# Performance work log

Measured on AMD Instinct MI355X. Metric: run time of the kernel, lower is better.

Reference implementation:

```python
import jax, jax.numpy as jnp
import numpy as np

T, B, I, H, O = 512, 64, 256, 512, 256

def setup_inputs() -> dict:
    key = jax.random.key(0)
    ks = jax.random.split(key, 7)
    s_ih = 1.0 / np.sqrt(H)
    return {
        "inputs": jax.random.normal(ks[0], (T, B, I), dtype=jnp.float32),
        "W_ih": jax.random.uniform(ks[1], (4 * H, I), minval=-s_ih, maxval=s_ih, dtype=jnp.float32),
        "W_hh": jax.random.uniform(ks[2], (4 * H, H), minval=-s_ih, maxval=s_ih, dtype=jnp.float32),
        "b_ih": jax.random.uniform(ks[3], (4 * H,), minval=-s_ih, maxval=s_ih, dtype=jnp.float32),
        "b_hh": jax.random.uniform(ks[4], (4 * H,), minval=-s_ih, maxval=s_ih, dtype=jnp.float32),
        "W_out": jax.random.uniform(ks[5], (O, H), minval=-s_ih, maxval=s_ih, dtype=jnp.float32),
        "b_out": jax.random.uniform(ks[6], (O,), minval=-s_ih, maxval=s_ih, dtype=jnp.float32),
    }

def reference(inputs, W_ih, W_hh, b_ih, b_hh, W_out, b_out):
    Bsz = inputs.shape[1]
    Hd = W_hh.shape[1]
    h0 = jnp.zeros((Bsz, Hd), dtype=inputs.dtype)
    c0 = jnp.zeros((Bsz, Hd), dtype=inputs.dtype)
    # Precompute input contribution for all timesteps in one big GEMM: [T,B,4H]
    x_gates = jnp.einsum('tbi,gi->tbg', inputs, W_ih) + b_ih + b_hh

    def step(carry, xg):
        h, c = carry
        gates = xg + h @ W_hh.T  # [B,4H]
        i, f, g, o = jnp.split(gates, 4, axis=-1)  # PyTorch LSTMCell gate order
        i = jax.nn.sigmoid(i)
        f = jax.nn.sigmoid(f)
        g = jnp.tanh(g)
        o = jax.nn.sigmoid(o)
        c_new = f * c + i * g
        h_new = o * jnp.tanh(c_new)
        return (h_new, c_new), h_new

    (h_T, c_T), hs = jax.lax.scan(step, (h0, c0), x_gates)
    # Output projection over all timesteps at once: [T,B,O]
    outputs = jnp.einsum('tbh,oh->tbo', hs, W_out) + b_out
    return (outputs, h_T, c_T)
```

## Files before the change

kernel.cpp:

```cpp
#include <hip/hip_runtime.h>
#include <hip/hip_bf16.h>

#define TLEN 512
#define BATCH 64
#define ISZ 256
#define HSZ 512
#define OSZ 256
#define G4 2048

typedef float f32x4 __attribute__((ext_vector_type(4)));
typedef short short8 __attribute__((ext_vector_type(8)));
typedef int int4v __attribute__((ext_vector_type(4)));

#define MFMA(a, b, c) __builtin_amdgcn_mfma_f32_16x16x32_bf16((a), (b), (c), 0, 0, 0)

__device__ __forceinline__ unsigned short f2bf(float x) {
    unsigned int u = __float_as_uint(x);
    u = (u + 0x7fffu + ((u >> 16) & 1u)) >> 16;
    return (unsigned short)u;
}
__device__ __forceinline__ float bf2f(unsigned short h) {
    return __uint_as_float(((unsigned int)h) << 16);
}
__device__ __forceinline__ float sigmoidf_(float x) { return 1.0f / (1.0f + __expf(-x)); }
__device__ __forceinline__ float tanhf_(float x) { return 1.0f - 2.0f / (__expf(2.0f * x) + 1.0f); }

__global__ void __launch_bounds__(512, 1) xg_gemm(
    const float* __restrict__ inp, const float* __restrict__ Wih,
    const float* __restrict__ b_ih, const float* __restrict__ b_hh,
    unsigned short* __restrict__ xg)
{
    __shared__ short8 blds[8][8][64];
    const int tid = threadIdx.x;
    {
        int row = tid >> 2;
        int kseg = (tid & 3) * 64;
        int nt = row >> 4, nn = row & 15;
        const float* src = Wih + (size_t)(blockIdx.y * 128 + row) * ISZ + kseg;
        for (int kk = 0; kk < 64; ++kk) {
            int k = kseg + kk;
            int kf = k >> 5, sub = k & 31;
            ((unsigned short*)&blds[nt][kf][((sub >> 3) << 4) | nn])[sub & 7] = f2bf(src[kk]);
        }
    }
    __syncthreads();
    const int wave = tid >> 6, lane = tid & 63;
    const int m0 = blockIdx.x * 128 + wave * 16;
    f32x4 acc[8];
    #pragma unroll
    for (int i = 0; i < 8; ++i) acc[i] = (f32x4){0.f, 0.f, 0.f, 0.f};
    const float* arow = inp + (size_t)(m0 + (lane & 15)) * ISZ + ((lane >> 4) * 8);
    #pragma unroll
    for (int kf = 0; kf < 8; ++kf) {
        f32x4 a0 = *(const f32x4*)(arow + kf * 32);
        f32x4 a1 = *(const f32x4*)(arow + kf * 32 + 4);
        short8 af;
        #pragma unroll
        for (int i = 0; i < 4; ++i) { af[i] = (short)f2bf(a0[i]); af[4 + i] = (short)f2bf(a1[i]); }
        #pragma unroll
        for (int nt = 0; nt < 8; ++nt)
            acc[nt] = MFMA(af, blds[nt][kf][lane], acc[nt]);
    }
    const int nn = lane & 15;
    #pragma unroll
    for (int nt = 0; nt < 8; ++nt) {
        int nc = blockIdx.y * 128 + nt * 16 + nn;
        float bias = b_ih[nc] + b_hh[nc];
        #pragma unroll
        for (int r = 0; r < 4; ++r) {
            int m = m0 + (lane >> 4) * 4 + r;
            xg[(size_t)m * G4 + nc] = f2bf(acc[nt][r] + bias);
        }
    }
}

__global__ void __attribute__((amdgpu_waves_per_eu(1, 1))) __launch_bounds__(256, 1) lstm_scan(
    const float* __restrict__ Whh, const unsigned short* __restrict__ xg,
    unsigned short* __restrict__ hs, unsigned int* __restrict__ hbuf,
    float* __restrict__ out_tail)
{
    __shared__ short8 wlds[4][16][64];
    const int wg = blockIdx.x, tid = threadIdx.x;
    const int wave = tid >> 6, lane = tid & 63;
    const int l15 = lane & 15, l4 = lane >> 4;
    const int col = wg * 16 + l15;

    {
        const int g = wave;
        const float* wrow = Whh + (size_t)(g * HSZ + wg * 16 + l15) * HSZ + l4 * 8;
        #pragma unroll
        for (int kf = 0; kf < 16; ++kf) {
            f32x4 w0 = *(const f32x4*)(wrow + kf * 32);
            f32x4 w1 = *(const f32x4*)(wrow + kf * 32 + 4);
            short8 f;
            #pragma unroll
            for (int e = 0; e < 4; ++e) { f[e] = (short)f2bf(w0[e]); f[4 + e] = (short)f2bf(w1[e]); }
            wlds[g][kf][lane] = f;
        }
    }
    __syncthreads();

    float cr[4] = {0.f, 0.f, 0.f, 0.f};
    const int mbase = wave * 16 + l4 * 4;

    #pragma unroll 1
    for (int t = 0; t < TLEN; ++t) {
        unsigned int xgv[4][4];
        {
            const char* x0 = (const char*)(xg + (size_t)(t * BATCH + mbase) * G4 + col);
            #pragma unroll
            for (int r = 0; r < 4; ++r) {
                const char* xr = x0 + r * (G4 * 2);
                asm volatile("global_load_ushort %0, %1, off offset:0"    : "=v"(xgv[0][r]) : "v"(xr));
                asm volatile("global_load_ushort %0, %1, off offset:1024" : "=v"(xgv[1][r]) : "v"(xr));
                asm volatile("global_load_ushort %0, %1, off offset:2048" : "=v"(xgv[2][r]) : "v"(xr));
                asm volatile("global_load_ushort %0, %1, off offset:3072" : "=v"(xgv[3][r]) : "v"(xr));
            }
        }

        f32x4 acc[4];
        #pragma unroll
        for (int g = 0; g < 4; ++g) acc[g] = (f32x4){0.f, 0.f, 0.f, 0.f};

        if (t > 0) {
            const unsigned tag = (unsigned)t;
            const char* hb = (const char*)hbuf + (t & 1) * 131072
                           + (size_t)(wave * 16 + l15) * 2048 + l4 * 32;
            int4v hv[32];
            while (true) {
                #pragma unroll
                for (int kf = 0; kf < 16; ++kf) {
                    asm volatile("global_load_dwordx4 %0, %1, off offset:%2 sc0 sc1"
                                 : "=&v"(hv[2 * kf])     : "v"(hb), "i"(kf * 128));
                    asm volatile("global_load_dwordx4 %0, %1, off offset:%2 sc0 sc1"
                                 : "=&v"(hv[2 * kf + 1]) : "v"(hb), "i"(kf * 128 + 16));
                }
                asm volatile("s_waitcnt vmcnt(0)" ::: "memory");
                __builtin_amdgcn_sched_barrier(0);
                unsigned bad = 0;
                #pragma unroll
                for (int w = 0; w < 32; ++w) {
                    bad |= (unsigned)(hv[w][0] ^ (int)tag);
                    bad |= (unsigned)(hv[w][1] ^ (int)tag);
                    bad |= (unsigned)(hv[w][2] ^ (int)tag);
                    bad |= (unsigned)(hv[w][3] ^ (int)tag);
                }
                if (__all((bad & 0xFFFFu) == 0)) break;
            }
            __builtin_amdgcn_sched_barrier(0);
            #pragma unroll
            for (int kf = 0; kf < 16; ++kf) {
                int4v w0 = hv[2 * kf], w1 = hv[2 * kf + 1];
                int4v f;
                f[0] = (int)(((unsigned)w0[0] >> 16) | ((unsigned)w0[1] & 0xFFFF0000u));
                f[1] = (int)(((unsigned)w0[2] >> 16) | ((unsigned)w0[3] & 0xFFFF0000u));
                f[2] = (int)(((unsigned)w1[0] >> 16) | ((unsigned)w1[1] & 0xFFFF0000u));
                f[3] = (int)(((unsigned)w1[2] >> 16) | ((unsigned)w1[3] & 0xFFFF0000u));
                short8 a = *(short8*)&f;
                acc[0] = MFMA(a, wlds[0][kf][lane], acc[0]);
                acc[1] = MFMA(a, wlds[1][kf][lane], acc[1]);
                acc[2] = MFMA(a, wlds[2][kf][lane], acc[2]);
                acc[3] = MFMA(a, wlds[3][kf][lane], acc[3]);
            }
        }
        asm volatile("s_waitcnt vmcnt(0)" ::: "memory");
        __builtin_amdgcn_sched_barrier(0);

        float hnv[4];
        #pragma unroll
        for (int r = 0; r < 4; ++r) {
            float iv = acc[0][r] + bf2f((unsigned short)xgv[0][r]);
            float fv2= acc[1][r] + bf2f((unsigned short)xgv[1][r]);
            float gv = acc[2][r] + bf2f((unsigned short)xgv[2][r]);
            float ov = acc[3][r] + bf2f((unsigned short)xgv[3][r]);
            float si = sigmoidf_(iv), sf = sigmoidf_(fv2), so = sigmoidf_(ov);
            float tg = tanhf_(gv);
            float cn = sf * cr[r] + si * tg;
            cr[r] = cn;
            hnv[r] = so * tanhf_(cn);
        }

        {
            const unsigned ptag = (unsigned)(t + 1);
            const unsigned pbase = ((unsigned)((t + 1) & 1)) * 32768u + (unsigned)col;
            #pragma unroll
            for (int r = 0; r < 4; ++r) {
                unsigned word = (((unsigned)f2bf(hnv[r])) << 16) | ptag;
                __hip_atomic_store(&hbuf[pbase + (unsigned)(mbase + r) * 512], word,
                                   __ATOMIC_RELAXED, __HIP_MEMORY_SCOPE_AGENT);
            }
        }

        #pragma unroll
        for (int r = 0; r < 4; ++r) {
            int m = mbase + r;
            hs[((size_t)t * BATCH + m) * HSZ + col] = f2bf(hnv[r]);
            if (t == TLEN - 1) {
                out_tail[(size_t)m * HSZ + col] = hnv[r];
                out_tail[(size_t)BATCH * HSZ + (size_t)m * HSZ + col] = cr[r];
            }
        }
    }
}

__global__ void __launch_bounds__(512, 1) out_gemm(
    const unsigned short* __restrict__ hs, const float* __restrict__ Wout,
    const float* __restrict__ b_out, float* __restrict__ out)
{
    __shared__ short8 blds[4][16][64];
    const int tid = threadIdx.x;
    {
        int row = tid >> 3;
        int kseg = (tid & 7) * 64;
        int nt = row >> 4, nn = row & 15;
        const float* src = Wout + (size_t)(blockIdx.y * 64 + row) * HSZ + kseg;
        for (int kk = 0; kk < 64; ++kk) {
            int k = kseg + kk;
            int kf = k >> 5, sub = k & 31;
            ((unsigned short*)&blds[nt][kf][((sub >> 3) << 4) | nn])[sub & 7] = f2bf(src[kk]);
        }
    }
    __syncthreads();
    const int wave = tid >> 6, lane = tid & 63;
    const int m0 = blockIdx.x * 128 + wave * 16;
    f32x4 acc[4];
    #pragma unroll
    for (int i = 0; i < 4; ++i) acc[i] = (f32x4){0.f, 0.f, 0.f, 0.f};
    const unsigned short* arow = hs + (size_t)(m0 + (lane & 15)) * HSZ + ((lane >> 4) * 8);
    #pragma unroll
    for (int kf = 0; kf < 16; ++kf) {
        short8 a = *(const short8*)(arow + kf * 32);
        #pragma unroll
        for (int nt = 0; nt < 4; ++nt)
            acc[nt] = MFMA(a, blds[nt][kf][lane], acc[nt]);
    }
    const int nn = lane & 15;
    #pragma unroll
    for (int nt = 0; nt < 4; ++nt) {
        int nc = blockIdx.y * 64 + nt * 16 + nn;
        float bias = b_out[nc];
        #pragma unroll
        for (int r = 0; r < 4; ++r) {
            int m = m0 + (lane >> 4) * 4 + r;
            out[(size_t)m * OSZ + nc] = acc[nt][r] + bias;
        }
    }
}

extern "C" void kernel_launch(void* const* d_in, const int* in_sizes, int n_in,
                              void* d_out, int out_size, void* d_ws, size_t ws_size,
                              hipStream_t stream)
{
    const float* inputs = (const float*)d_in[0];
    const float* W_ih  = (const float*)d_in[1];
    const float* W_hh  = (const float*)d_in[2];
    const float* b_ih  = (const float*)d_in[3];
    const float* b_hh  = (const float*)d_in[4];
    const float* W_out = (const float*)d_in[5];
    const float* b_out = (const float*)d_in[6];
    float* out = (float*)d_out;

    char* ws = (char*)d_ws;
    unsigned short* xg = (unsigned short*)ws;
    unsigned short* hs = (unsigned short*)(ws + 134217728);
    unsigned int* hbuf = (unsigned int*)(ws + 134217728 + 33554432);

    xg_gemm<<<dim3(256, 16), 512, 0, stream>>>(inputs, W_ih, b_ih, b_hh, xg);

    float* out_tail = out + (size_t)TLEN * BATCH * OSZ;
    const float* whh_p = W_hh;
    const unsigned short* xg_p = xg;
    unsigned short* hs_p = hs;
    unsigned int* hbuf_p = hbuf;
    float* tail_p = out_tail;
    void* scan_args[] = { &whh_p, &xg_p, &hs_p, &hbuf_p, &tail_p };
    hipLaunchCooperativeKernel((void*)lstm_scan, dim3(32), dim3(256), scan_args, 0, stream);

    out_gemm<<<dim3(256, 4), 512, 0, stream>>>(hs, W_out, b_out, out);
}
```

Before: 4.105 ms.

## Re-layout xg gate buffer per column for vectorized loads and trim tag checks

```diff
diff --git a/kernel.cpp b/kernel.cpp
--- a/kernel.cpp
+++ b/kernel.cpp
@@ -10,6 +10,7 @@
 
 typedef float f32x4 __attribute__((ext_vector_type(4)));
 typedef short short8 __attribute__((ext_vector_type(8)));
+typedef int int2v __attribute__((ext_vector_type(2)));
 typedef int int4v __attribute__((ext_vector_type(4)));
 
 #define MFMA(a, b, c) __builtin_amdgcn_mfma_f32_16x16x32_bf16((a), (b), (c), 0, 0, 0)
@@ -62,15 +63,17 @@
             acc[nt] = MFMA(af, blds[nt][kf][lane], acc[nt]);
     }
     const int nn = lane & 15;
+    const int mf = m0 + (lane >> 4) * 4;
+    const int tt = mf >> 6, bb = mf & 63;
     #pragma unroll
     for (int nt = 0; nt < 8; ++nt) {
         int nc = blockIdx.y * 128 + nt * 16 + nn;
         float bias = b_ih[nc] + b_hh[nc];
-        #pragma unroll
-        for (int r = 0; r < 4; ++r) {
-            int m = m0 + (lane >> 4) * 4 + r;
-            xg[(size_t)m * G4 + nc] = f2bf(acc[nt][r] + bias);
-        }
+        int colc = nc & 511, gate = nc >> 9;
+        unsigned lo = (unsigned)f2bf(acc[nt][0] + bias) | ((unsigned)f2bf(acc[nt][1] + bias) << 16);
+        unsigned hi = (unsigned)f2bf(acc[nt][2] + bias) | ((unsigned)f2bf(acc[nt][3] + bias) << 16);
+        int2v w; w[0] = (int)lo; w[1] = (int)hi;
+        *(int2v*)((char*)xg + (size_t)(tt * 512 + colc) * 512 + gate * 128 + bb * 2) = w;
     }
 }
 
@@ -105,17 +108,16 @@
 
     #pragma unroll 1
     for (int t = 0; t < TLEN; ++t) {
-        unsigned int xgv[4][4];
+        int2v xv[4];
         {
-            const char* x0 = (const char*)(xg + (size_t)(t * BATCH + mbase) * G4 + col);
-            #pragma unroll
-            for (int r = 0; r < 4; ++r) {
-                const char* xr = x0 + r * (G4 * 2);
-                asm volatile("global_load_ushort %0, %1, off offset:0"    : "=v"(xgv[0][r]) : "v"(xr));
-                asm volatile("global_load_ushort %0, %1, off offset:1024" : "=v"(xgv[1][r]) : "v"(xr));
-                asm volatile("global_load_ushort %0, %1, off offset:2048" : "=v"(xgv[2][r]) : "v"(xr));
-                asm volatile("global_load_ushort %0, %1, off offset:3072" : "=v"(xgv[3][r]) : "v"(xr));
-            }
+            const char* xb = (const char*)xg + (size_t)(t * 512 + col) * 512 + mbase * 2;
+            asm volatile(
+                "global_load_dwordx2 %0, %4, off offset:0\n\t"
+                "global_load_dwordx2 %1, %4, off offset:128\n\t"
+                "global_load_dwordx2 %2, %4, off offset:256\n\t"
+                "global_load_dwordx2 %3, %4, off offset:384"
+                : "=&v"(xv[0]), "=&v"(xv[1]), "=&v"(xv[2]), "=&v"(xv[3])
+                : "v"(xb) : "memory");
         }
 
         f32x4 acc[4];
@@ -128,23 +130,54 @@
                            + (size_t)(wave * 16 + l15) * 2048 + l4 * 32;
             int4v hv[32];
             while (true) {
-                #pragma unroll
-                for (int kf = 0; kf < 16; ++kf) {
-                    asm volatile("global_load_dwordx4 %0, %1, off offset:%2 sc0 sc1"
-                                 : "=&v"(hv[2 * kf])     : "v"(hb), "i"(kf * 128));
-                    asm volatile("global_load_dwordx4 %0, %1, off offset:%2 sc0 sc1"
-                                 : "=&v"(hv[2 * kf + 1]) : "v"(hb), "i"(kf * 128 + 16));
-                }
+                asm volatile(
+                    "global_load_dwordx4 %0, %32, off offset:0 sc0 sc1\n\t"
+                    "global_load_dwordx4 %1, %32, off offset:16 sc0 sc1\n\t"
+                    "global_load_dwordx4 %2, %32, off offset:128 sc0 sc1\n\t"
+                    "global_load_dwordx4 %3, %32, off offset:144 sc0 sc1\n\t"
+                    "global_load_dwordx4 %4, %32, off offset:256 sc0 sc1\n\t"
+                    "global_load_dwordx4 %5, %32, off offset:272 sc0 sc1\n\t"
+                    "global_load_dwordx4 %6, %32, off offset:384 sc0 sc1\n\t"
+                    "global_load_dwordx4 %7, %32, off offset:400 sc0 sc1\n\t"
+                    "global_load_dwordx4 %8, %32, off offset:512 sc0 sc1\n\t"
+                    "global_load_dwordx4 %9, %32, off offset:528 sc0 sc1\n\t"
+                    "global_load_dwordx4 %10, %32, off offset:640 sc0 sc1\n\t"
+                    "global_load_dwordx4 %11, %32, off offset:656 sc0 sc1\n\t"
+                    "global_load_dwordx4 %12, %32, off offset:768 sc0 sc1\n\t"
+                    "global_load_dwordx4 %13, %32, off offset:784 sc0 sc1\n\t"
+                    "global_load_dwordx4 %14, %32, off offset:896 sc0 sc1\n\t"
+                    "global_load_dwordx4 %15, %32, off offset:912 sc0 sc1\n\t"
+                    "global_load_dwordx4 %16, %32, off offset:1024 sc0 sc1\n\t"
+                    "global_load_dwordx4 %17, %32, off offset:1040 sc0 sc1\n\t"
+                    "global_load_dwordx4 %18, %32, off offset:1152 sc0 sc1\n\t"
+                    "global_load_dwordx4 %19, %32, off offset:1168 sc0 sc1\n\t"
+                    "global_load_dwordx4 %20, %32, off offset:1280 sc0 sc1\n\t"
+                    "global_load_dwordx4 %21, %32, off offset:1296 sc0 sc1\n\t"
+                    "global_load_dwordx4 %22, %32, off offset:1408 sc0 sc1\n\t"
+                    "global_load_dwordx4 %23, %32, off offset:1424 sc0 sc1\n\t"
+                    "global_load_dwordx4 %24, %32, off offset:1536 sc0 sc1\n\t"
+                    "global_load_dwordx4 %25, %32, off offset:1552 sc0 sc1\n\t"
+                    "global_load_dwordx4 %26, %32, off offset:1664 sc0 sc1\n\t"
+                    "global_load_dwordx4 %27, %32, off offset:1680 sc0 sc1\n\t"
+                    "global_load_dwordx4 %28, %32, off offset:1792 sc0 sc1\n\t"
+                    "global_load_dwordx4 %29, %32, off offset:1808 sc0 sc1\n\t"
+                    "global_load_dwordx4 %30, %32, off offset:1920 sc0 sc1\n\t"
+                    "global_load_dwordx4 %31, %32, off offset:1936 sc0 sc1"
+                    : "=&v"(hv[0]), "=&v"(hv[1]), "=&v"(hv[2]), "=&v"(hv[3]),
+                      "=&v"(hv[4]), "=&v"(hv[5]), "=&v"(hv[6]), "=&v"(hv[7]),
+                      "=&v"(hv[8]), "=&v"(hv[9]), "=&v"(hv[10]), "=&v"(hv[11]),
+                      "=&v"(hv[12]), "=&v"(hv[13]), "=&v"(hv[14]), "=&v"(hv[15]),
+                      "=&v"(hv[16]), "=&v"(hv[17]), "=&v"(hv[18]), "=&v"(hv[19]),
+                      "=&v"(hv[20]), "=&v"(hv[21]), "=&v"(hv[22]), "=&v"(hv[23]),
+                      "=&v"(hv[24]), "=&v"(hv[25]), "=&v"(hv[26]), "=&v"(hv[27]),
+                      "=&v"(hv[28]), "=&v"(hv[29]), "=&v"(hv[30]), "=&v"(hv[31])
+                    : "v"(hb) : "memory");
                 asm volatile("s_waitcnt vmcnt(0)" ::: "memory");
                 __builtin_amdgcn_sched_barrier(0);
                 unsigned bad = 0;
                 #pragma unroll
-                for (int w = 0; w < 32; ++w) {
-                    bad |= (unsigned)(hv[w][0] ^ (int)tag);
-                    bad |= (unsigned)(hv[w][1] ^ (int)tag);
-                    bad |= (unsigned)(hv[w][2] ^ (int)tag);
-                    bad |= (unsigned)(hv[w][3] ^ (int)tag);
-                }
+                for (int w = 0; w < 32; ++w)
+                    bad |= (unsigned)hv[w][0] ^ tag;
                 if (__all((bad & 0xFFFFu) == 0)) break;
             }
             __builtin_amdgcn_sched_barrier(0);
@@ -162,17 +195,21 @@
                 acc[2] = MFMA(a, wlds[2][kf][lane], acc[2]);
                 acc[3] = MFMA(a, wlds[3][kf][lane], acc[3]);
             }
-        }
-        asm volatile("s_waitcnt vmcnt(0)" ::: "memory");
-        __builtin_amdgcn_sched_barrier(0);
+        } else {
+            asm volatile("s_waitcnt vmcnt(0)" ::: "memory");
+            __builtin_amdgcn_sched_barrier(0);
+        }
 
         float hnv[4];
         #pragma unroll
         for (int r = 0; r < 4; ++r) {
-            float iv = acc[0][r] + bf2f((unsigned short)xgv[0][r]);
-            float fv2= acc[1][r] + bf2f((unsigned short)xgv[1][r]);
-            float gv = acc[2][r] + bf2f((unsigned short)xgv[2][r]);
-            float ov = acc[3][r] + bf2f((unsigned short)xgv[3][r]);
+            unsigned w0 = (unsigned)xv[0][r >> 1], w1 = (unsigned)xv[1][r >> 1];
+            unsigned w2 = (unsigned)xv[2][r >> 1], w3 = (unsigned)xv[3][r >> 1];
+            int sh = (r & 1) * 16;
+            float iv = acc[0][r] + bf2f((unsigned short)(w0 >> sh));
+            float fv2= acc[1][r] + bf2f((unsigned short)(w1 >> sh));
+            float gv = acc[2][r] + bf2f((unsigned short)(w2 >> sh));
+            float ov = acc[3][r] + bf2f((unsigned short)(w3 >> sh));
             float si = sigmoidf_(iv), sf = sigmoidf_(fv2), so = sigmoidf_(ov);
             float tg = tanhf_(gv);
             float cn = sf * cr[r] + si * tg;
@@ -195,7 +232,11 @@
         for (int r = 0; r < 4; ++r) {
             int m = mbase + r;
             hs[((size_t)t * BATCH + m) * HSZ + col] = f2bf(hnv[r]);
-            if (t == TLEN - 1) {
+        }
+        if (t == TLEN - 1) {
+            #pragma unroll
+            for (int r = 0; r < 4; ++r) {
+                int m = mbase + r;
                 out_tail[(size_t)m * HSZ + col] = hnv[r];
                 out_tail[(size_t)BATCH * HSZ + (size_t)m * HSZ + col] = cr[r];
             }
```

Result: slower. 4.228 ms (+3.0%).
